# Kernel optimization log

Measured on AMD Instinct MI355X. Metric: run time of the kernel, lower is better.

Reference implementation:

```python
import jax, jax.numpy as jnp
import numpy as np

EPS = 1e-7  # perplexity log epsilon (matches compute_perplexity)


def _vq_step(carry, cb):
    """One QuantizeEMAReset layer (eval mode) applied to the current residual.

    carry: (residual (B,C,T), quantized_out (B,C,T)); cb: (K, C) codebook.
    """
    residual, quantized_out = carry
    B, C, T = residual.shape
    # preprocess: (B,C,T) -> (B*T, C)
    xf = jnp.transpose(residual, (0, 2, 1)).reshape(-1, C)
    dist = (jnp.sum(xf * xf, axis=1, keepdims=True)
            - 2.0 * (xf @ cb.T)
            + jnp.sum(cb * cb, axis=1))           # (B*T, K)
    idx = jnp.argmin(dist, axis=1)                # (B*T,)
    xd = cb[idx]                                  # dequantize gather (B*T, C)
    # commitment loss: mse(x, x_d.detach())
    commit = jnp.mean((xf - jax.lax.stop_gradient(xd)) ** 2)
    # perplexity from code-usage histogram
    counts = jnp.zeros((cb.shape[0],), xf.dtype).at[idx].add(1.0)
    prob = counts / xf.shape[0]
    perplexity = jnp.exp(-jnp.sum(prob * jnp.log(prob + EPS)))
    # straight-through estimator
    xd_st = xf + jax.lax.stop_gradient(xd - xf)
    quantized = jnp.transpose(xd_st.reshape(B, T, C), (0, 2, 1))  # (B,C,T)
    residual = residual - jax.lax.stop_gradient(quantized)
    quantized_out = quantized_out + quantized
    return (residual, quantized_out), (idx.reshape(B, T), commit, perplexity)


def _forward(x, codebooks):
    init = (x, jnp.zeros_like(x))
    (_, qout), (idxs, losses, perps) = jax.lax.scan(_vq_step, init, codebooks)
    all_indices = jnp.transpose(idxs, (1, 2, 0))  # (B, T, Q)
    return qout, all_indices, jnp.mean(losses), jnp.mean(perps)


def setup_inputs() -> dict:
    key = jax.random.key(0)
    kx, kc = jax.random.split(key)
    B, C, T = 64, 512, 256
    Q, K = 6, 1024
    x = jax.random.normal(kx, (B, C, T), dtype=jnp.float32)
    codebooks = jax.random.normal(kc, (Q, K, C), dtype=jnp.float32)
    return {"x": x, "codebooks": codebooks}


def reference(x, codebooks):
    # returns (quantized_out, all_indices, mean_commit_loss, mean_perplexity)
    return _forward(x, codebooks)
```

## Files before the change

kernel.cpp:

```cpp
#include <hip/hip_runtime.h>

typedef short bf16x8 __attribute__((ext_vector_type(8)));
typedef float f32x4  __attribute__((ext_vector_type(4)));

#define NB   64
#define NT   256
#define NC   512
#define NK   1024
#define NQ   6
#define NROWS (NB*NT)
#define QOUT_ELEMS 8388608
#define IDX_ELEMS  98304
#define DELTA 0.5f
#define CAP  64

#define WS_CAND   0
#define WS_CCNT   0x800000
#define WS_BIDX   0x810000
#define WS_COUNTS 0x820000
#define WS_CSUM   0x821000
#define WS_CMEAN  0x821020
#define WS_PERP   0x821040
#define WS_DONE   0x821060
#define WS_CBN    0x822000
#define WS_XHI    0x830000
#define WS_CBHI   (WS_XHI + 16777216)

__device__ __forceinline__ unsigned short f2bf(float f) {
    unsigned u = __float_as_uint(f);
    return (unsigned short)((u + 0x7FFFu + ((u >> 16) & 1u)) >> 16);
}

__device__ __forceinline__ void load_lds16(const unsigned short* g, unsigned short* l) {
    __builtin_amdgcn_global_load_lds(
        (const __attribute__((address_space(1))) unsigned int*)g,
        (__attribute__((address_space(3))) unsigned int*)l,
        16, 0, 0);
}

__device__ __forceinline__ unsigned lds_addr(const unsigned short* p) {
    return (unsigned)(unsigned long long)
        (const __attribute__((address_space(3))) unsigned short*)p;
}

#define DSR(d, b, IMM) \
    asm volatile("ds_read_b128 %0, %1 offset:" #IMM : "=v"(d) : "v"(b))

__global__ __launch_bounds__(256) void vq_cvt_cb(const float* __restrict__ cb,
                                                 unsigned short* __restrict__ cbhi,
                                                 float* __restrict__ cbn) {
    int lane = threadIdx.x & 63, wid = threadIdx.x >> 6;
    int code = blockIdx.x * 4 + wid;
    int layer = code >> 10, cin = code & 1023;
    const float* row = cb + (size_t)code * NC;
    float4 v0 = *(const float4*)(row + lane * 8);
    float4 v1 = *(const float4*)(row + lane * 8 + 4);
    float vs[8] = {v0.x, v0.y, v0.z, v0.w, v1.x, v1.y, v1.z, v1.w};
    ushort4 a, b;
    unsigned short* ap = &a.x; unsigned short* bp = &b.x;
    float s = 0.f;
    #pragma unroll
    for (int j = 0; j < 4; ++j) {
        s += vs[j] * vs[j] + vs[j+4] * vs[j+4];
        ap[j] = f2bf(vs[j]); bp[j] = f2bf(vs[j+4]);
    }
    size_t o = (size_t)layer * NK * NC
             + (((size_t)(lane >> 3) * NK + cin) << 6)
             + (((lane & 7) ^ (cin & 7)) << 3);
    *(ushort4*)(cbhi + o) = a; *(ushort4*)(cbhi + o + 4) = b;
    #pragma unroll
    for (int off = 32; off; off >>= 1) s += __shfl_down(s, off, 64);
    if (lane == 0) cbn[code] = 0.5f * s;
}

__global__ __launch_bounds__(256) void vq_cvt_x(const float* __restrict__ x,
                                                unsigned short* __restrict__ xh,
                                                unsigned int* __restrict__ candcnt,
                                                unsigned int* __restrict__ done) {
    __shared__ unsigned short hs[64][72];
    int bx = blockIdx.x;
    int b = bx >> 5, tt = (bx >> 3) & 3, kk = bx & 7;
    int c0 = kk << 6, t0 = tt << 6, tid = threadIdx.x;
    if (kk == 0 && tid < 64) candcnt[b * 256 + t0 + tid] = 0u;
    if (bx == 0 && tid == 0) *done = 0u;
    const float* base = x + (size_t)b * (NC * NT) + t0;
    #pragma unroll
    for (int i = 0; i < 4; ++i) {
        int f = tid + (i << 8);
        int c_l = f >> 4, t4 = f & 15;
        float4 v = *(const float4*)(base + (size_t)(c0 + c_l) * NT + (t4 << 2));
        ushort4 hh;
        hh.x = f2bf(v.x); hh.y = f2bf(v.y); hh.z = f2bf(v.z); hh.w = f2bf(v.w);
        *(ushort4*)&hs[c_l][t4 << 2] = hh;
    }
    __syncthreads();
    int row0 = b * NT + t0;
    #pragma unroll
    for (int i = 0; i < 4; ++i) {
        int f = tid + (i << 8);
        int r_l = f >> 4, c4 = f & 15;
        ushort4 hh;
        hh.x = hs[c4*4+0][r_l]; hh.y = hs[c4*4+1][r_l];
        hh.z = hs[c4*4+2][r_l]; hh.w = hs[c4*4+3][r_l];
        int cq = c4 >> 1, h = c4 & 1;
        *(ushort4*)(xh + (((size_t)kk * NROWS + row0 + r_l) << 6)
                       + ((cq ^ (r_l & 7)) << 3) + (h << 2)) = hh;
    }
}

__global__ __launch_bounds__(512, 2) void vq_dist(
    const unsigned short* __restrict__ xh, const unsigned short* __restrict__ ch,
    const float* __restrict__ cbn,
    unsigned int* __restrict__ cand, unsigned int* __restrict__ candcnt,
    unsigned int* __restrict__ counts, float* __restrict__ commit_slot)
{
    extern __shared__ unsigned short smem[];
    const int rb = blockIdx.x, cg = blockIdx.y, tid = threadIdx.x;
    if (rb == 0 && cg == 0) {
        for (int i = tid; i < NK; i += 512) counts[i] = 0u;
        if (tid == 0) *commit_slot = 0.f;
    }
    const int wave = tid >> 6, lane = tid & 63;
    const int idx16 = lane & 15, quad = lane >> 4;
    const int wm = wave >> 2, wn = wave & 3;
    const int m0 = rb * 256, n0 = cg * 256;

    const unsigned short* gsrc = (wave < 4) ? xh : ch;
    const int tbase = (wave < 4) ? m0 : n0;
    const size_t strideK = (size_t)((wave < 4) ? NROWS : NK) << 6;
    const unsigned short* gp = gsrc + ((size_t)tbase << 6) + ((wave & 3) << 12) + lane * 8;
    unsigned short* lp0 = &smem[((wave < 4) ? 0 : 16384) + ((wave & 3) << 12) + lane * 8];

    unsigned aB[2][2], bB[2][2];
    #pragma unroll
    for (int ks = 0; ks < 2; ++ks) {
        int slot = ((quad + 4 * ks) ^ (idx16 & 7)) << 3;
        aB[0][ks] = lds_addr(&smem[(wm * 128 + idx16) * 64 + slot]);
        bB[0][ks] = lds_addr(&smem[16384 + (wn * 64 + idx16) * 64 + slot]);
        aB[1][ks] = aB[0][ks] + 65536u;
        bB[1][ks] = bB[0][ks] + 65536u;
    }

    f32x4 acc[8][4];
    #pragma unroll
    for (int mt = 0; mt < 8; ++mt)
        #pragma unroll
        for (int nt = 0; nt < 4; ++nt) acc[mt][nt] = (f32x4){0.f, 0.f, 0.f, 0.f};

    #pragma unroll
    for (int i = 0; i < 8; ++i)
        load_lds16(gp + i * 512, lp0 + i * 512);

    #define KS_BODY(ABASE, BBASE)                                              \
    {                                                                          \
        bf16x8 a[8], b[4];                                                     \
        DSR(a[0], ABASE, 0);     DSR(a[1], ABASE, 2048);                       \
        DSR(a[2], ABASE, 4096);  DSR(a[3], ABASE, 6144);                       \
        DSR(a[4], ABASE, 8192);  DSR(a[5], ABASE, 10240);                      \
        DSR(a[6], ABASE, 12288); DSR(a[7], ABASE, 14336);                      \
        DSR(b[0], BBASE, 0);     DSR(b[1], BBASE, 2048);                       \
        DSR(b[2], BBASE, 4096);  DSR(b[3], BBASE, 6144);                       \
        asm volatile("s_waitcnt lgkmcnt(0)" ::: "memory");                     \
        __builtin_amdgcn_sched_barrier(0);                                     \
        __builtin_amdgcn_s_setprio(1);                                         \
        _Pragma("unroll")                                                      \
        for (int mt = 0; mt < 8; ++mt)                                         \
            _Pragma("unroll")                                                  \
            for (int nt = 0; nt < 4; ++nt)                                     \
                acc[mt][nt] = __builtin_amdgcn_mfma_f32_16x16x32_bf16(         \
                    a[mt], b[nt], acc[mt][nt], 0, 0, 0);                       \
        __builtin_amdgcn_s_setprio(0);                                         \
        __builtin_amdgcn_sched_barrier(0);                                     \
    }

    #pragma unroll
    for (int k = 0; k < 8; ++k) {
        const int BUF = k & 1;
        if (k < 7) {
            unsigned short* lp = lp0 + ((BUF ^ 1) << 15);
            const unsigned short* g = gp + (size_t)(k + 1) * strideK;
            #pragma unroll
            for (int i = 0; i < 8; ++i)
                load_lds16(g + i * 512, lp + i * 512);
            asm volatile("s_waitcnt vmcnt(8)" ::: "memory");
        } else {
            asm volatile("s_waitcnt vmcnt(0)" ::: "memory");
        }
        __builtin_amdgcn_s_barrier();
        __builtin_amdgcn_sched_barrier(0);
        KS_BODY(aB[BUF][0], bB[BUF][0]);
        KS_BODY(aB[BUF][1], bB[BUF][1]);
        __builtin_amdgcn_s_barrier();
        __builtin_amdgcn_sched_barrier(0);
    }
    #undef KS_BODY

    float cn[4]; int ng[4];
    #pragma unroll
    for (int nt = 0; nt < 4; ++nt) {
        ng[nt] = n0 + wn * 64 + nt * 16 + idx16;
        cn[nt] = cbn[ng[nt]];
    }
    #pragma unroll
    for (int mt = 0; mt < 8; ++mt) {
        #pragma unroll
        for (int r = 0; r < 4; ++r) {
            float sc[4];
            float m = 3.402823466e38f;
            #pragma unroll
            for (int nt = 0; nt < 4; ++nt) {
                sc[nt] = cn[nt] - acc[mt][nt][r];
                m = fminf(m, sc[nt]);
            }
            #pragma unroll
            for (int sft = 1; sft < 16; sft <<= 1)
                m = fminf(m, __shfl_xor(m, sft, 64));
            m += DELTA;
            const int row = m0 + wm * 128 + mt * 16 + quad * 4 + r;
            #pragma unroll
            for (int nt = 0; nt < 4; ++nt) {
                if (sc[nt] <= m) {
                    unsigned slot = atomicAdd(&candcnt[row], 1u);
                    if (slot < (unsigned)CAP)
                        ((uint2*)cand)[(size_t)row * CAP + slot] =
                            make_uint2((unsigned)ng[nt], __float_as_uint(sc[nt]));
                }
            }
        }
    }
}

__global__ __launch_bounds__(256) void vq_rescore(
    const float* __restrict__ src,
    const float* __restrict__ cb, const float* __restrict__ cbn,
    const unsigned int* __restrict__ cand, const unsigned int* __restrict__ candcnt,
    int* __restrict__ best_idx, float* __restrict__ out_idx,
    unsigned int* __restrict__ counts, int q)
{
    __shared__ float xl[16][512];
    const int tid = threadIdx.x;
    const int b = blockIdx.x >> 4, t0 = (blockIdx.x & 15) << 4;
    const float* base = src + (size_t)b * (NC * NT) + t0;
    #pragma unroll
    for (int i = 0; i < 8; ++i) {
        int f = tid + (i << 8);
        int c = f >> 2, t4 = f & 3;
        float4 v = *(const float4*)(base + (size_t)c * NT + (t4 << 2));
        xl[(t4 << 2) + 0][c] = v.x; xl[(t4 << 2) + 1][c] = v.y;
        xl[(t4 << 2) + 2][c] = v.z; xl[(t4 << 2) + 3][c] = v.w;
    }
    __syncthreads();
    const int w = tid >> 6, lane = tid & 63;
    const int row0 = b * NT + t0;
    const uint2* cp = (const uint2*)cand;
    for (int rr = 0; rr < 4; ++rr) {
        const int tl = w * 4 + rr;
        const int row = row0 + tl;
        float4 xa = *(const float4*)&xl[tl][lane << 3];
        float4 xb = *(const float4*)&xl[tl][(lane << 3) + 4];
        int n = (int)candcnt[row]; if (n > CAP) n = CAP;
        uint2 pr = make_uint2(0x7FFFFFFFu, 0x7F800000u);
        if (lane < n) pr = cp[(size_t)row * CAP + lane];
        float scf = __uint_as_float(pr.y);
        float rmin = scf;
        #pragma unroll
        for (int off = 1; off < 64; off <<= 1) rmin = fminf(rmin, __shfl_xor(rmin, off, 64));
        unsigned long long msk = __ballot(scf <= rmin + DELTA);
        float bs = 3.402823466e38f; int bi = 0x7FFFFFFF;
        while (msk) {
            int j = (int)__ffsll(msk) - 1; msk &= msk - 1;
            int code = __shfl((int)pr.x, j, 64);
            const float* cr = cb + (size_t)code * NC + (lane << 3);
            float4 ca = *(const float4*)cr;
            float4 cc = *(const float4*)(cr + 4);
            float s = xa.x*ca.x + xa.y*ca.y + xa.z*ca.z + xa.w*ca.w
                    + xb.x*cc.x + xb.y*cc.y + xb.z*cc.z + xb.w*cc.w;
            #pragma unroll
            for (int off = 1; off < 64; off <<= 1) s += __shfl_xor(s, off, 64);
            s = cbn[code] - s;
            if (s < bs || (s == bs && code < bi)) { bs = s; bi = code; }
        }
        if (lane == 0) {
            best_idx[row] = bi;
            out_idx[(size_t)row * NQ + q] = (float)bi;
            atomicAdd(&counts[bi], 1u);
        }
    }
}

__global__ __launch_bounds__(256) void vq_update(
    const float* __restrict__ src,
    float* __restrict__ dst,
    const float* __restrict__ cb,
    const int* __restrict__ best_idx,
    unsigned short* __restrict__ xh,
    unsigned int* __restrict__ candcnt,
    unsigned int* __restrict__ counts,
    float* __restrict__ csum, float* __restrict__ cmean, float* __restrict__ perp,
    float* __restrict__ out_tail, unsigned int* __restrict__ done, int q)
{
    const int rb = blockIdx.x, tid = threadIdx.x;
    const int b = rb >> 2, t0 = (rb & 3) << 6;
    const int row0 = rb * 64;
    __shared__ int s_idx[64];
    __shared__ __align__(16) float qt[64][68];
    __shared__ float wsum[4];
    __shared__ unsigned int lastflag;
    if (tid < 64) {
        s_idx[tid] = best_idx[row0 + tid];
        candcnt[row0 + tid] = 0u;
    }
    __syncthreads();
    float cs = 0.f;
    const size_t base = (size_t)b * (NC * NT) + t0;
    for (int ct = 0; ct < 8; ++ct) {
        if (ct) __syncthreads();
        #pragma unroll
        for (int i = 0; i < 4; ++i) {
            int f = tid + (i << 8);
            int r = f >> 4, cf = f & 15;
            float4 v = *(const float4*)(cb + (size_t)s_idx[r] * NC + ct * 64 + (cf << 2));
            qt[(cf << 2) + 0][r] = v.x;
            qt[(cf << 2) + 1][r] = v.y;
            qt[(cf << 2) + 2][r] = v.z;
            qt[(cf << 2) + 3][r] = v.w;
        }
        __syncthreads();
        #pragma unroll
        for (int i = 0; i < 4; ++i) {
            int f = tid + (i << 8);
            int c_l = f >> 4, tf = f & 15;
            size_t o = base + (size_t)(ct * 64 + c_l) * NT + (tf << 2);
            float4 r4 = *(const float4*)(src + o);
            float4 q4 = *(const float4*)&qt[c_l][tf << 2];
            float4 n;
            n.x = r4.x - q4.x; n.y = r4.y - q4.y; n.z = r4.z - q4.z; n.w = r4.w - q4.w;
            *(float4*)(dst + o) = n;
            *(float4*)&qt[c_l][tf << 2] = n;
            cs += n.x*n.x + n.y*n.y + n.z*n.z + n.w*n.w;
        }
        __syncthreads();
        #pragma unroll
        for (int i = 0; i < 4; ++i) {
            int f = tid + (i << 8);
            int r_l = f >> 4, c4 = f & 15;
            ushort4 hh;
            hh.x = f2bf(qt[c4*4+0][r_l]); hh.y = f2bf(qt[c4*4+1][r_l]);
            hh.z = f2bf(qt[c4*4+2][r_l]); hh.w = f2bf(qt[c4*4+3][r_l]);
            int cq = c4 >> 1, h = c4 & 1;
            *(ushort4*)(xh + (((size_t)ct * NROWS + row0 + r_l) << 6)
                           + ((cq ^ (r_l & 7)) << 3) + (h << 2)) = hh;
        }
    }
    #pragma unroll
    for (int off = 32; off; off >>= 1) cs += __shfl_down(cs, off, 64);
    if ((tid & 63) == 0) wsum[tid >> 6] = cs;
    __syncthreads();
    if (tid == 0) {
        atomicAdd(&csum[q], wsum[0] + wsum[1] + wsum[2] + wsum[3]);
        __threadfence();
        lastflag = atomicAdd(done, 1u);
    }
    __syncthreads();
    if (lastflag == 255u) {
        float v = 0.f;
        for (int i = tid; i < NK; i += 256) {
            float p = (float)atomicAdd(&counts[i], 0u) * (1.f / (float)NROWS);
            v += p * logf(p + 1e-7f);
        }
        #pragma unroll
        for (int off = 32; off; off >>= 1) v += __shfl_down(v, off, 64);
        if ((tid & 63) == 0) wsum[tid >> 6] = v;
        __syncthreads();
        if (tid == 0) {
            float S = wsum[0] + wsum[1] + wsum[2] + wsum[3];
            perp[q]  = expf(-S);
            cmean[q] = atomicAdd(&csum[q], 0.f) * (1.f / ((float)NROWS * (float)NC));
            if (q == NQ - 1) {
                float mc = 0.f, mp = 0.f;
                for (int i = 0; i < NQ; ++i) { mc += cmean[i]; mp += perp[i]; }
                out_tail[0] = mc / (float)NQ;
                out_tail[1] = mp / (float)NQ;
            }
            *done = 0u;
        }
    }
}

__global__ void vq_finalize(const float* __restrict__ x, float* __restrict__ res, int n4) {
    int i = blockIdx.x * blockDim.x + threadIdx.x;
    if (i < n4) {
        float4 a = ((const float4*)x)[i];
        float4 r = ((float4*)res)[i];
        float4 o;
        o.x = a.x - r.x; o.y = a.y - r.y; o.z = a.z - r.z; o.w = a.w - r.w;
        ((float4*)res)[i] = o;
    }
}

extern "C" void kernel_launch(void* const* d_in, const int* in_sizes, int n_in,
                              void* d_out, int out_size, void* d_ws, size_t ws_size,
                              hipStream_t stream) {
    static int inited = 0;
    if (!inited) {
        (void)hipFuncSetAttribute((const void*)vq_dist,
                                  hipFuncAttributeMaxDynamicSharedMemorySize, 131072);
        inited = 1;
    }
    const float* x  = (const float*)d_in[0];
    const float* cb = (const float*)d_in[1];
    float* out      = (float*)d_out;
    float* res      = out;
    float* out_idx  = out + QOUT_ELEMS;
    float* out_tail = out + QOUT_ELEMS + IDX_ELEMS;
    char* ws = (char*)d_ws;
    unsigned int* cand    = (unsigned int*)(ws + WS_CAND);
    unsigned int* candcnt = (unsigned int*)(ws + WS_CCNT);
    int*          bidx    = (int*)(ws + WS_BIDX);
    unsigned int* counts  = (unsigned int*)(ws + WS_COUNTS);
    float* csum  = (float*)(ws + WS_CSUM);
    float* cmean = (float*)(ws + WS_CMEAN);
    float* perp  = (float*)(ws + WS_PERP);
    unsigned int* done = (unsigned int*)(ws + WS_DONE);
    float* cbn   = (float*)(ws + WS_CBN);
    unsigned short* xh   = (unsigned short*)(ws + WS_XHI);
    unsigned short* cbhi = (unsigned short*)(ws + WS_CBHI);

    vq_cvt_cb<<<1536, 256, 0, stream>>>(cb, cbhi, cbn);
    vq_cvt_x<<<2048, 256, 0, stream>>>(x, xh, candcnt, done);
    for (int q = 0; q < NQ; ++q) {
        const float* src = (q == 0) ? x : res;
        const float* cbq = cb + (size_t)q * NK * NC;
        vq_dist<<<dim3(64, 4), 512, 131072, stream>>>(
            xh, cbhi + (size_t)q * NK * NC, cbn + q * NK,
            cand, candcnt, counts, csum + q);
        vq_rescore<<<1024, 256, 0, stream>>>(src, cbq, cbn + q * NK, cand, candcnt,
                                             bidx, out_idx, counts, q);
        vq_update<<<256, 256, 0, stream>>>(src, res, cbq, bidx, xh, candcnt,
                                           counts, csum, cmean, perp, out_tail, done, q);
    }
    vq_finalize<<<8192, 256, 0, stream>>>(x, res, QOUT_ELEMS / 4);
}
```

Baseline: 761.6 us.

## Fuse rescore, residual update and finalize into one kernel per layer

Merges the rescore and update kernels so the residual tile already staged in shared memory is reused to compute the new residual, commitment loss and bf16 copy. This avoids a second read of the residual and codebook rows and the best-index round trip. The final x minus residual step moves into the last layer's pass, so the separate finalize kernel goes away. It also pads the shared tile to reduce bank conflicts and skips the bf16 write on the last layer. The trade-off is a larger per-block shared footprint and the completion counter now assumes 1024 blocks.

```diff
diff --git a/kernel.cpp b/kernel.cpp
--- a/kernel.cpp
+++ b/kernel.cpp
@@ -230,14 +230,21 @@
     }
 }
 
-__global__ __launch_bounds__(256) void vq_rescore(
+__global__ __launch_bounds__(256) void vq_fused(
     const float* __restrict__ src,
+    float* __restrict__ dst,
+    const float* __restrict__ x,
     const float* __restrict__ cb, const float* __restrict__ cbn,
-    const unsigned int* __restrict__ cand, const unsigned int* __restrict__ candcnt,
-    int* __restrict__ best_idx, float* __restrict__ out_idx,
-    unsigned int* __restrict__ counts, int q)
+    const unsigned int* __restrict__ cand, unsigned int* __restrict__ candcnt,
+    float* __restrict__ out_idx, unsigned int* __restrict__ counts,
+    unsigned short* __restrict__ xh,
+    float* __restrict__ csum, float* __restrict__ cmean, float* __restrict__ perp,
+    float* __restrict__ out_tail, unsigned int* __restrict__ done, int q)
 {
-    __shared__ float xl[16][512];
+    __shared__ float xl[16][516];
+    __shared__ int s_bi[16];
+    __shared__ float wsum[4];
+    __shared__ unsigned int lastflag;
     const int tid = threadIdx.x;
     const int b = blockIdx.x >> 4, t0 = (blockIdx.x & 15) << 4;
     const float* base = src + (size_t)b * (NC * NT) + t0;
@@ -253,6 +260,7 @@
     const int w = tid >> 6, lane = tid & 63;
     const int row0 = b * NT + t0;
     const uint2* cp = (const uint2*)cand;
+    float cs = 0.f;
     for (int rr = 0; rr < 4; ++rr) {
         const int tl = w * 4 + rr;
         const int row = row0 + tl;
@@ -281,88 +289,55 @@
             if (s < bs || (s == bs && code < bi)) { bs = s; bi = code; }
         }
         if (lane == 0) {
-            best_idx[row] = bi;
             out_idx[(size_t)row * NQ + q] = (float)bi;
             atomicAdd(&counts[bi], 1u);
-        }
-    }
-}
-
-__global__ __launch_bounds__(256) void vq_update(
-    const float* __restrict__ src,
-    float* __restrict__ dst,
-    const float* __restrict__ cb,
-    const int* __restrict__ best_idx,
-    unsigned short* __restrict__ xh,
-    unsigned int* __restrict__ candcnt,
-    unsigned int* __restrict__ counts,
-    float* __restrict__ csum, float* __restrict__ cmean, float* __restrict__ perp,
-    float* __restrict__ out_tail, unsigned int* __restrict__ done, int q)
-{
-    const int rb = blockIdx.x, tid = threadIdx.x;
-    const int b = rb >> 2, t0 = (rb & 3) << 6;
-    const int row0 = rb * 64;
-    __shared__ int s_idx[64];
-    __shared__ __align__(16) float qt[64][68];
-    __shared__ float wsum[4];
-    __shared__ unsigned int lastflag;
-    if (tid < 64) {
-        s_idx[tid] = best_idx[row0 + tid];
-        candcnt[row0 + tid] = 0u;
-    }
+            candcnt[row] = 0u;
+        }
+        const float* cr = cb + (size_t)bi * NC + (lane << 3);
+        float4 ca = *(const float4*)cr;
+        float4 cc = *(const float4*)(cr + 4);
+        float4 n0, n1;
+        n0.x = xa.x - ca.x; n0.y = xa.y - ca.y; n0.z = xa.z - ca.z; n0.w = xa.w - ca.w;
+        n1.x = xb.x - cc.x; n1.y = xb.y - cc.y; n1.z = xb.z - cc.z; n1.w = xb.w - cc.w;
+        cs += n0.x*n0.x + n0.y*n0.y + n0.z*n0.z + n0.w*n0.w
+            + n1.x*n1.x + n1.y*n1.y + n1.z*n1.z + n1.w*n1.w;
+        *(float4*)&xl[tl][lane << 3] = n0;
+        *(float4*)&xl[tl][(lane << 3) + 4] = n1;
+        if (q < NQ - 1) {
+            int kk = lane >> 3, cq = lane & 7;
+            size_t o = (((size_t)kk * NROWS + row) << 6) + ((cq ^ (row & 7)) << 3);
+            ushort4 h0, h1;
+            h0.x = f2bf(n0.x); h0.y = f2bf(n0.y); h0.z = f2bf(n0.z); h0.w = f2bf(n0.w);
+            h1.x = f2bf(n1.x); h1.y = f2bf(n1.y); h1.z = f2bf(n1.z); h1.w = f2bf(n1.w);
+            *(ushort4*)(xh + o) = h0; *(ushort4*)(xh + o + 4) = h1;
+        }
+    }
+    #pragma unroll
+    for (int off = 32; off; off >>= 1) cs += __shfl_down(cs, off, 64);
+    if (lane == 0) wsum[w] = cs;
     __syncthreads();
-    float cs = 0.f;
-    const size_t base = (size_t)b * (NC * NT) + t0;
-    for (int ct = 0; ct < 8; ++ct) {
-        if (ct) __syncthreads();
-        #pragma unroll
-        for (int i = 0; i < 4; ++i) {
-            int f = tid + (i << 8);
-            int r = f >> 4, cf = f & 15;
-            float4 v = *(const float4*)(cb + (size_t)s_idx[r] * NC + ct * 64 + (cf << 2));
-            qt[(cf << 2) + 0][r] = v.x;
-            qt[(cf << 2) + 1][r] = v.y;
-            qt[(cf << 2) + 2][r] = v.z;
-            qt[(cf << 2) + 3][r] = v.w;
-        }
-        __syncthreads();
-        #pragma unroll
-        for (int i = 0; i < 4; ++i) {
-            int f = tid + (i << 8);
-            int c_l = f >> 4, tf = f & 15;
-            size_t o = base + (size_t)(ct * 64 + c_l) * NT + (tf << 2);
-            float4 r4 = *(const float4*)(src + o);
-            float4 q4 = *(const float4*)&qt[c_l][tf << 2];
-            float4 n;
-            n.x = r4.x - q4.x; n.y = r4.y - q4.y; n.z = r4.z - q4.z; n.w = r4.w - q4.w;
-            *(float4*)(dst + o) = n;
-            *(float4*)&qt[c_l][tf << 2] = n;
-            cs += n.x*n.x + n.y*n.y + n.z*n.z + n.w*n.w;
-        }
-        __syncthreads();
-        #pragma unroll
-        for (int i = 0; i < 4; ++i) {
-            int f = tid + (i << 8);
-            int r_l = f >> 4, c4 = f & 15;
-            ushort4 hh;
-            hh.x = f2bf(qt[c4*4+0][r_l]); hh.y = f2bf(qt[c4*4+1][r_l]);
-            hh.z = f2bf(qt[c4*4+2][r_l]); hh.w = f2bf(qt[c4*4+3][r_l]);
-            int cq = c4 >> 1, h = c4 & 1;
-            *(ushort4*)(xh + (((size_t)ct * NROWS + row0 + r_l) << 6)
-                           + ((cq ^ (r_l & 7)) << 3) + (h << 2)) = hh;
-        }
-    }
-    #pragma unroll
-    for (int off = 32; off; off >>= 1) cs += __shfl_down(cs, off, 64);
-    if ((tid & 63) == 0) wsum[tid >> 6] = cs;
-    __syncthreads();
+    const size_t ob = (size_t)b * (NC * NT) + t0;
+    #pragma unroll
+    for (int i = 0; i < 8; ++i) {
+        int f = tid + (i << 8);
+        int c = f >> 2, tq = f & 3;
+        float4 o;
+        o.x = xl[(tq << 2) + 0][c]; o.y = xl[(tq << 2) + 1][c];
+        o.z = xl[(tq << 2) + 2][c]; o.w = xl[(tq << 2) + 3][c];
+        size_t idx = ob + (size_t)c * NT + (tq << 2);
+        if (q == NQ - 1) {
+            float4 xv = *(const float4*)(x + idx);
+            o.x = xv.x - o.x; o.y = xv.y - o.y; o.z = xv.z - o.z; o.w = xv.w - o.w;
+        }
+        *(float4*)(dst + idx) = o;
+    }
     if (tid == 0) {
         atomicAdd(&csum[q], wsum[0] + wsum[1] + wsum[2] + wsum[3]);
         __threadfence();
         lastflag = atomicAdd(done, 1u);
     }
     __syncthreads();
-    if (lastflag == 255u) {
+    if (lastflag == 1023u) {
         float v = 0.f;
         for (int i = tid; i < NK; i += 256) {
             float p = (float)atomicAdd(&counts[i], 0u) * (1.f / (float)NROWS);
@@ -387,17 +362,6 @@
     }
 }
 
-__global__ void vq_finalize(const float* __restrict__ x, float* __restrict__ res, int n4) {
-    int i = blockIdx.x * blockDim.x + threadIdx.x;
-    if (i < n4) {
-        float4 a = ((const float4*)x)[i];
-        float4 r = ((float4*)res)[i];
-        float4 o;
-        o.x = a.x - r.x; o.y = a.y - r.y; o.z = a.z - r.z; o.w = a.w - r.w;
-        ((float4*)res)[i] = o;
-    }
-}
-
 extern "C" void kernel_launch(void* const* d_in, const int* in_sizes, int n_in,
                               void* d_out, int out_size, void* d_ws, size_t ws_size,
                               hipStream_t stream) {
@@ -416,7 +380,6 @@
     char* ws = (char*)d_ws;
     unsigned int* cand    = (unsigned int*)(ws + WS_CAND);
     unsigned int* candcnt = (unsigned int*)(ws + WS_CCNT);
-    int*          bidx    = (int*)(ws + WS_BIDX);
     unsigned int* counts  = (unsigned int*)(ws + WS_COUNTS);
     float* csum  = (float*)(ws + WS_CSUM);
     float* cmean = (float*)(ws + WS_CMEAN);
@@ -434,10 +397,8 @@
         vq_dist<<<dim3(64, 4), 512, 131072, stream>>>(
             xh, cbhi + (size_t)q * NK * NC, cbn + q * NK,
             cand, candcnt, counts, csum + q);
-        vq_rescore<<<1024, 256, 0, stream>>>(src, cbq, cbn + q * NK, cand, candcnt,
-                                             bidx, out_idx, counts, q);
-        vq_update<<<256, 256, 0, stream>>>(src, res, cbq, bidx, xh, candcnt,
-                                           counts, csum, cmean, perp, out_tail, done, q);
-    }
-    vq_finalize<<<8192, 256, 0, stream>>>(x, res, QOUT_ELEMS / 4);
-}
+        vq_fused<<<1024, 256, 0, stream>>>(src, res, x, cbq, cbn + q * NK,
+                                           cand, candcnt, out_idx, counts, xh,
+                                           csum, cmean, perp, out_tail, done, q);
+    }
+}
```

Measured after the change: 897.0 us. 1.18x slower.
